# Optimization experiments

Measured on AMD Instinct MI355X. Metric: run time of the kernel, lower is better.

The kernel has to match this reference:

```python
import jax, jax.numpy as jnp
import numpy as np

N_NODES = 50000
N_PAIRS = 800000
D = 64          # node feature dim
N_BASIS = 8     # basis functions per pair


def setup_inputs() -> dict:
    key = jax.random.key(0)
    k1, k2, k3, k4, k5, k6 = jax.random.split(key, 6)
    p1 = jax.random.normal(k1, (N_NODES, D), dtype=jnp.float32)
    pair_i = jax.random.randint(k2, (N_PAIRS,), 0, N_NODES, dtype=jnp.int64)
    pair_j = jax.random.randint(k3, (N_PAIRS,), 0, N_NODES, dtype=jnp.int64)
    basis = jax.random.normal(k4, (N_PAIRS, N_BASIS), dtype=jnp.float32)
    # bias-free MLP: 64 -> 256 -> 512 (= D * N_BASIS), scaled init
    W1 = jax.random.normal(k5, (D, 256), dtype=jnp.float32) / np.sqrt(D)
    W2 = jax.random.normal(k6, (256, D * N_BASIS), dtype=jnp.float32) / np.sqrt(256.0)
    return {"p1": p1, "pair_i": pair_i, "pair_j": pair_j, "basis": basis,
            "W1": W1, "W2": W2}


def reference(p1, pair_i, pair_j, basis, W1, W2):
    # gather node features for both ends of each pair and sum -> [n_pairs, D]
    inter = p1[pair_i] + p1[pair_j]
    # bias-free FeedForward with tanh between layers
    h = jnp.tanh(inter @ W1)          # [n_pairs, 256]
    h = h @ W2                        # [n_pairs, D * N_BASIS]
    h = h.reshape(-1, p1.shape[-1], basis.shape[-1])  # [n_pairs, D, n_basis]
    out = jnp.einsum('icb,ib->ic', h, basis)          # [n_pairs, D]
    return out[:, None, :]            # [n_pairs, 1, D]
```

## Files before the change

### kernel.cpp

```cpp
#include <hip/hip_runtime.h>

typedef unsigned short u16;
typedef unsigned int   u32;
typedef __bf16 bf16x8 __attribute__((ext_vector_type(8)));
typedef float  f32x4  __attribute__((ext_vector_type(4)));
typedef float  f32x2  __attribute__((ext_vector_type(2)));
typedef unsigned short u16x8 __attribute__((ext_vector_type(8)));
typedef unsigned int   u32x2 __attribute__((ext_vector_type(2)));

#define PPB 160

__device__ __forceinline__ u16 f2bf(float f){
  union { float f; u32 i; } v; v.f = f;
  u32 u = v.i;
  u += 0x7fffu + ((u >> 16) & 1u);
  return (u16)(u >> 16);
}
__device__ __forceinline__ float tanh_fast(float x){
  x = fminf(fmaxf(x, -12.f), 12.f);
  float t = __builtin_amdgcn_exp2f(x * 2.885390081777926815f);
  return (t - 1.f) * __builtin_amdgcn_rcpf(t + 1.f);
}

__global__ __launch_bounds__(256) void transpose_cast_k(
    const float* __restrict__ in, u16* __restrict__ out, int R, int C)
{
  __shared__ u16 tile[64][65];
  const int tx = threadIdx.x & 63;
  const int ty = threadIdx.x >> 6;
  const int c0 = blockIdx.x * 64;
  const int r0 = blockIdx.y * 64;
#pragma unroll
  for (int rr = 0; rr < 16; ++rr){
    int r = ty + rr * 4;
    tile[r][tx] = f2bf(in[(size_t)(r0 + r) * C + c0 + tx]);
  }
  __syncthreads();
#pragma unroll
  for (int rr = 0; rr < 16; ++rr){
    int r = ty + rr * 4;
    out[(size_t)(c0 + r) * R + r0 + tx] = tile[tx][r];
  }
}

__global__ __launch_bounds__(256) void w2_block_k(
    const float* __restrict__ in, u16* __restrict__ out)
{
  __shared__ float tile[32][65];
  const int kk = blockIdx.x;
  const int n0 = blockIdx.y * 64;
  const int t  = threadIdx.x;
  {
    int r  = t >> 3;
    int c8 = t & 7;
    const float* src = in + (size_t)(kk*32 + r)*512 + n0 + c8*8;
    f32x4 v0 = *(const f32x4*)src;
    f32x4 v1 = *(const f32x4*)(src + 4);
#pragma unroll
    for (int e = 0; e < 4; ++e){
      tile[r][c8*8 + e]     = v0[e];
      tile[r][c8*8 + 4 + e] = v1[e];
    }
  }
  __syncthreads();
  {
    int c = t >> 2, part = t & 3;
    u16x8 o;
#pragma unroll
    for (int e = 0; e < 8; ++e) o[e] = f2bf(tile[part*8 + e][c]);
    *(u16x8*)(out + ((size_t)kk*512 + n0 + c)*32 + part*8) = o;
  }
}

__global__ __launch_bounds__(1024, 4) void pilayer_kernel(
    const float* __restrict__ p1,
    const int* __restrict__ pair_i,
    const int* __restrict__ pair_j,
    const float* __restrict__ basis,
    const u16* __restrict__ w1t,
    const u16* __restrict__ w2b,
    float* __restrict__ out,
    int n_pairs)
{
  extern __shared__ __align__(16) u16 smem[];
  u16* sh_h     = smem;
  u16* sh_inter = smem + PPB * 256;

  const int tid  = threadIdx.x;
  const int blk  = blockIdx.x;
  const int lane = tid & 63;
  const int w    = tid >> 6;
  const int m16  = lane & 15;
  const int q    = lane >> 4;
  const int sw   = m16 & 7;

  bf16x8 awf[8][2];
#pragma unroll
  for (int kk = 0; kk < 8; ++kk)
#pragma unroll
    for (int nt = 0; nt < 2; ++nt)
      awf[kk][nt] = *(const bf16x8*)(
          w2b + ((size_t)kk*512 + w*32 + nt*16 + m16)*32 + q*8);
  __builtin_amdgcn_sched_barrier(0);

  for (int u = tid; u < PPB * 8; u += 1024){
    int m   = u >> 3;
    int seg = u & 7;
    int p   = blk * PPB + m;
    if (p >= n_pairs) p = n_pairs - 1;
    const f32x4* pi = (const f32x4*)(p1 + (size_t)pair_i[p] * 64 + seg * 8);
    const f32x4* pj = (const f32x4*)(p1 + (size_t)pair_j[p] * 64 + seg * 8);
    f32x4 a0 = pi[0], a1 = pi[1];
    f32x4 c0 = pj[0], c1 = pj[1];
    u16x8 r;
#pragma unroll
    for (int e = 0; e < 4; ++e){
      r[e]     = f2bf(a0[e] + c0[e]);
      r[e + 4] = f2bf(a1[e] + c1[e]);
    }
    *(u16x8*)(sh_inter + m * 64 + ((seg ^ (m & 7)) * 8)) = r;
  }
  __syncthreads();

  {
    const u16* arow = w1t + (size_t)(w*16 + m16)*64 + q*8;
    bf16x8 af0 = *(const bf16x8*)(arow);
    bf16x8 af1 = *(const bf16x8*)(arow + 32);
    const int cw = (w*2 + (q >> 1)) ^ sw;
    for (int mt1 = 0; mt1 < PPB/16; ++mt1){
      const u16* irow = sh_inter + (size_t)(mt1*16 + m16) * 64;
      bf16x8 b0 = *(const bf16x8*)(irow + (q ^ sw) * 8);
      bf16x8 b1 = *(const bf16x8*)(irow + ((q + 4) ^ sw) * 8);
      f32x4 acc = {0.f, 0.f, 0.f, 0.f};
      acc = __builtin_amdgcn_mfma_f32_16x16x32_bf16(af0, b0, acc, 0, 0, 0);
      acc = __builtin_amdgcn_mfma_f32_16x16x32_bf16(af1, b1, acc, 0, 0, 0);
      u32 lo = (u32)f2bf(tanh_fast(acc[0])) | ((u32)f2bf(tanh_fast(acc[1])) << 16);
      u32 hi = (u32)f2bf(tanh_fast(acc[2])) | ((u32)f2bf(tanh_fast(acc[3])) << 16);
      u32x2 pk = {lo, hi};
      *(u32x2*)(sh_h + (size_t)(mt1*16 + m16)*256 + cw*8 + (q & 1)*4) = pk;
    }
  }
  __syncthreads();

  for (int mt = 0; mt < PPB/16; ++mt){
    const int row = mt*16 + m16;
    const int mg  = blk * PPB + row;
    const int mgc = (mg < n_pairs) ? mg : (n_pairs - 1);
    f32x4 bb = *(const f32x4*)(basis + (size_t)mgc*8 + (q & 1)*4);

    const u16* hbase = sh_h + (size_t)row * 256;
    f32x4 acc0 = {0.f, 0.f, 0.f, 0.f};
    f32x4 acc1 = {0.f, 0.f, 0.f, 0.f};

    bf16x8 bh = *(const bf16x8*)(hbase + (q ^ sw) * 8);
#pragma unroll
    for (int kk = 0; kk < 8; ++kk){
      bf16x8 bhn;
      if (kk < 7) bhn = *(const bf16x8*)(hbase + ((((kk + 1)*4 + q) ^ sw) * 8));
      acc0 = __builtin_amdgcn_mfma_f32_16x16x32_bf16(awf[kk][0], bh, acc0, 0, 0, 0);
      acc1 = __builtin_amdgcn_mfma_f32_16x16x32_bf16(awf[kk][1], bh, acc1, 0, 0, 0);
      bh = bhn;
    }

#pragma unroll
    for (int nt = 0; nt < 2; ++nt){
      f32x4 a = (nt == 0) ? acc0 : acc1;
      float s = a[0]*bb[0] + a[1]*bb[1] + a[2]*bb[2] + a[3]*bb[3];
      s += __shfl_xor(s, 16);
      float v2 = __shfl_xor(s, 32);
      if (q == 0 && mg < n_pairs){
        f32x2 pk = {s, v2};
        *(f32x2*)(out + (size_t)mg*64 + w*4 + nt*2) = pk;
      }
    }
  }
}

extern "C" void kernel_launch(void* const* d_in, const int* in_sizes, int n_in,
                              void* d_out, int out_size, void* d_ws, size_t ws_size,
                              hipStream_t stream)
{
  const float* p1    = (const float*)d_in[0];
  const int*   pi    = (const int*)d_in[1];
  const int*   pj    = (const int*)d_in[2];
  const float* basis = (const float*)d_in[3];
  const float* W1    = (const float*)d_in[4];
  const float* W2    = (const float*)d_in[5];
  float* out = (float*)d_out;

  u16* w1t = (u16*)d_ws;
  u16* w2b = w1t + 64 * 256;

  const int n_pairs = in_sizes[1];
  const int lds_bytes = (PPB * 256 + PPB * 64) * (int)sizeof(u16);

  static int attr_done = 0;
  if (!attr_done){
    hipFuncSetAttribute((const void*)pilayer_kernel,
                        hipFuncAttributeMaxDynamicSharedMemorySize, lds_bytes);
    attr_done = 1;
  }

  transpose_cast_k<<<dim3(4, 1), 256, 0, stream>>>(W1, w1t, 64, 256);
  w2_block_k<<<dim3(8, 8), 256, 0, stream>>>(W2, w2b);

  const int blocks = (n_pairs + PPB - 1) / PPB;
  pilayer_kernel<<<blocks, 1024, lds_bytes, stream>>>(
      p1, pi, pj, basis, w1t, w2b, out, n_pairs);
}
```

Before: 585.2 us.

## Process multiple pair chunks per block with double-buffered prefetched gathers

Each block now loops over five 128-pair chunks instead of handling one 160-pair chunk. While the second GEMM runs on the current chunk, it prefetches the next chunk's indices and node-feature gathers into a second LDS buffer. The W1 and W2 fragments held in registers are loaded once per block and reused across all chunks. The h-buffer swizzle is widened to a 4-bit XOR to reduce LDS bank conflicts. The cost is more registers for the prefetched data, an extra input buffer in LDS, and fewer blocks to hide latency with.

```diff
diff --git a/kernel.cpp b/kernel.cpp
--- a/kernel.cpp
+++ b/kernel.cpp
@@ -8,7 +8,8 @@
 typedef unsigned short u16x8 __attribute__((ext_vector_type(8)));
 typedef unsigned int   u32x2 __attribute__((ext_vector_type(2)));
 
-#define PPB 160
+#define PPB 128
+#define CPB 5
 
 __device__ __forceinline__ u16 f2bf(float f){
   union { float f; u32 i; } v; v.f = f;
@@ -83,8 +84,9 @@
     int n_pairs)
 {
   extern __shared__ __align__(16) u16 smem[];
-  u16* sh_h     = smem;
-  u16* sh_inter = smem + PPB * 256;
+  u16* sh_h  = smem;
+  u16* sh_i0 = smem + PPB * 256;
+  u16* sh_i1 = sh_i0 + PPB * 64;
 
   const int tid  = threadIdx.x;
   const int blk  = blockIdx.x;
@@ -92,7 +94,8 @@
   const int w    = tid >> 6;
   const int m16  = lane & 15;
   const int q    = lane >> 4;
-  const int sw   = m16 & 7;
+  const int sw3  = m16 & 7;
+  const int cw   = (w*2 + (q >> 1)) ^ m16;
 
   bf16x8 awf[8][2];
 #pragma unroll
@@ -101,36 +104,51 @@
     for (int nt = 0; nt < 2; ++nt)
       awf[kk][nt] = *(const bf16x8*)(
           w2b + ((size_t)kk*512 + w*32 + nt*16 + m16)*32 + q*8);
+  const u16* arow = w1t + (size_t)(w*16 + m16)*64 + q*8;
+  bf16x8 af0 = *(const bf16x8*)(arow);
+  bf16x8 af1 = *(const bf16x8*)(arow + 32);
   __builtin_amdgcn_sched_barrier(0);
 
-  for (int u = tid; u < PPB * 8; u += 1024){
-    int m   = u >> 3;
-    int seg = u & 7;
-    int p   = blk * PPB + m;
+  const int pbase = blk * CPB * PPB;
+  const int m_g   = tid >> 3;
+  const int seg_g = tid & 7;
+
+  {
+    int p = pbase + m_g;
     if (p >= n_pairs) p = n_pairs - 1;
-    const f32x4* pi = (const f32x4*)(p1 + (size_t)pair_i[p] * 64 + seg * 8);
-    const f32x4* pj = (const f32x4*)(p1 + (size_t)pair_j[p] * 64 + seg * 8);
-    f32x4 a0 = pi[0], a1 = pi[1];
-    f32x4 c0 = pj[0], c1 = pj[1];
+    const float* si = p1 + (size_t)pair_i[p]*64 + seg_g*8;
+    const float* sj = p1 + (size_t)pair_j[p]*64 + seg_g*8;
+    f32x4 a0 = ((const f32x4*)si)[0], a1 = ((const f32x4*)si)[1];
+    f32x4 b0 = ((const f32x4*)sj)[0], b1 = ((const f32x4*)sj)[1];
     u16x8 r;
 #pragma unroll
     for (int e = 0; e < 4; ++e){
-      r[e]     = f2bf(a0[e] + c0[e]);
-      r[e + 4] = f2bf(a1[e] + c1[e]);
-    }
-    *(u16x8*)(sh_inter + m * 64 + ((seg ^ (m & 7)) * 8)) = r;
+      r[e]     = f2bf(a0[e] + b0[e]);
+      r[e + 4] = f2bf(a1[e] + b1[e]);
+    }
+    *(u16x8*)(sh_i0 + m_g*64 + ((seg_g ^ (m_g & 7)) * 8)) = r;
   }
   __syncthreads();
 
-  {
-    const u16* arow = w1t + (size_t)(w*16 + m16)*64 + q*8;
-    bf16x8 af0 = *(const bf16x8*)(arow);
-    bf16x8 af1 = *(const bf16x8*)(arow + 32);
-    const int cw = (w*2 + (q >> 1)) ^ sw;
+  u16* sin_cur = sh_i0;
+  u16* sin_nxt = sh_i1;
+  int nxt_i = 0, nxt_j = 0;
+
+  for (int t = 0; t < CPB; ++t){
+    const int pb = pbase + t * PPB;
+    const bool pf = (t + 1 < CPB);
+
+    if (pf){
+      int pn = pb + PPB + m_g;
+      if (pn >= n_pairs) pn = n_pairs - 1;
+      nxt_i = pair_i[pn];
+      nxt_j = pair_j[pn];
+      asm volatile("" : "+v"(nxt_i), "+v"(nxt_j));
+    }
     for (int mt1 = 0; mt1 < PPB/16; ++mt1){
-      const u16* irow = sh_inter + (size_t)(mt1*16 + m16) * 64;
-      bf16x8 b0 = *(const bf16x8*)(irow + (q ^ sw) * 8);
-      bf16x8 b1 = *(const bf16x8*)(irow + ((q + 4) ^ sw) * 8);
+      const u16* irow = sin_cur + (size_t)(mt1*16 + m16) * 64;
+      bf16x8 b0 = *(const bf16x8*)(irow + ((q ^ sw3) * 8));
+      bf16x8 b1 = *(const bf16x8*)(irow + (((q + 4) ^ sw3) * 8));
       f32x4 acc = {0.f, 0.f, 0.f, 0.f};
       acc = __builtin_amdgcn_mfma_f32_16x16x32_bf16(af0, b0, acc, 0, 0, 0);
       acc = __builtin_amdgcn_mfma_f32_16x16x32_bf16(af1, b1, acc, 0, 0, 0);
@@ -139,40 +157,61 @@
       u32x2 pk = {lo, hi};
       *(u32x2*)(sh_h + (size_t)(mt1*16 + m16)*256 + cw*8 + (q & 1)*4) = pk;
     }
-  }
-  __syncthreads();
-
-  for (int mt = 0; mt < PPB/16; ++mt){
-    const int row = mt*16 + m16;
-    const int mg  = blk * PPB + row;
-    const int mgc = (mg < n_pairs) ? mg : (n_pairs - 1);
-    f32x4 bb = *(const f32x4*)(basis + (size_t)mgc*8 + (q & 1)*4);
-
-    const u16* hbase = sh_h + (size_t)row * 256;
-    f32x4 acc0 = {0.f, 0.f, 0.f, 0.f};
-    f32x4 acc1 = {0.f, 0.f, 0.f, 0.f};
-
-    bf16x8 bh = *(const bf16x8*)(hbase + (q ^ sw) * 8);
-#pragma unroll
-    for (int kk = 0; kk < 8; ++kk){
-      bf16x8 bhn;
-      if (kk < 7) bhn = *(const bf16x8*)(hbase + ((((kk + 1)*4 + q) ^ sw) * 8));
-      acc0 = __builtin_amdgcn_mfma_f32_16x16x32_bf16(awf[kk][0], bh, acc0, 0, 0, 0);
-      acc1 = __builtin_amdgcn_mfma_f32_16x16x32_bf16(awf[kk][1], bh, acc1, 0, 0, 0);
-      bh = bhn;
-    }
-
-#pragma unroll
-    for (int nt = 0; nt < 2; ++nt){
-      f32x4 a = (nt == 0) ? acc0 : acc1;
-      float s = a[0]*bb[0] + a[1]*bb[1] + a[2]*bb[2] + a[3]*bb[3];
-      s += __shfl_xor(s, 16);
-      float v2 = __shfl_xor(s, 32);
-      if (q == 0 && mg < n_pairs){
-        f32x2 pk = {s, v2};
-        *(f32x2*)(out + (size_t)mg*64 + w*4 + nt*2) = pk;
+    __syncthreads();
+
+    f32x4 gi0, gi1, gj0, gj1;
+    if (pf){
+      const float* si = p1 + (size_t)(u32)nxt_i*64 + seg_g*8;
+      const float* sj = p1 + (size_t)(u32)nxt_j*64 + seg_g*8;
+      gi0 = ((const f32x4*)si)[0]; gi1 = ((const f32x4*)si)[1];
+      gj0 = ((const f32x4*)sj)[0]; gj1 = ((const f32x4*)sj)[1];
+      asm volatile("" : "+v"(gi0), "+v"(gi1), "+v"(gj0), "+v"(gj1));
+    }
+
+    for (int mt = 0; mt < PPB/16; ++mt){
+      const int row = mt*16 + m16;
+      const int mg  = pb + row;
+      const int mgc = (mg < n_pairs) ? mg : (n_pairs - 1);
+      f32x4 bb = *(const f32x4*)(basis + (size_t)mgc*8 + (q & 1)*4);
+
+      const u16* hbase = sh_h + (size_t)row * 256;
+      f32x4 acc0 = {0.f, 0.f, 0.f, 0.f};
+      f32x4 acc1 = {0.f, 0.f, 0.f, 0.f};
+
+      bf16x8 bh = *(const bf16x8*)(hbase + ((q ^ m16) * 8));
+#pragma unroll
+      for (int kk = 0; kk < 8; ++kk){
+        bf16x8 bhn;
+        if (kk < 7) bhn = *(const bf16x8*)(hbase + ((((kk + 1)*4 + q) ^ m16) * 8));
+        acc0 = __builtin_amdgcn_mfma_f32_16x16x32_bf16(awf[kk][0], bh, acc0, 0, 0, 0);
+        acc1 = __builtin_amdgcn_mfma_f32_16x16x32_bf16(awf[kk][1], bh, acc1, 0, 0, 0);
+        bh = bhn;
       }
-    }
+
+#pragma unroll
+      for (int nt = 0; nt < 2; ++nt){
+        f32x4 a = (nt == 0) ? acc0 : acc1;
+        float s = a[0]*bb[0] + a[1]*bb[1] + a[2]*bb[2] + a[3]*bb[3];
+        s += __shfl_xor(s, 16);
+        float v2 = __shfl_xor(s, 32);
+        if (q == 0 && mg < n_pairs){
+          f32x2 pk = {s, v2};
+          *(f32x2*)(out + (size_t)mg*64 + w*4 + nt*2) = pk;
+        }
+      }
+    }
+
+    if (pf){
+      u16x8 r;
+#pragma unroll
+      for (int e = 0; e < 4; ++e){
+        r[e]     = f2bf(gi0[e] + gj0[e]);
+        r[e + 4] = f2bf(gi1[e] + gj1[e]);
+      }
+      *(u16x8*)(sin_nxt + m_g*64 + ((seg_g ^ (m_g & 7)) * 8)) = r;
+    }
+    __syncthreads();
+    u16* tmp = sin_cur; sin_cur = sin_nxt; sin_nxt = tmp;
   }
 }
 
@@ -192,7 +231,7 @@
   u16* w2b = w1t + 64 * 256;
 
   const int n_pairs = in_sizes[1];
-  const int lds_bytes = (PPB * 256 + PPB * 64) * (int)sizeof(u16);
+  const int lds_bytes = (PPB * 256 + 2 * PPB * 64) * (int)sizeof(u16);
 
   static int attr_done = 0;
   if (!attr_done){
@@ -204,7 +243,8 @@
   transpose_cast_k<<<dim3(4, 1), 256, 0, stream>>>(W1, w1t, 64, 256);
   w2_block_k<<<dim3(8, 8), 256, 0, stream>>>(W2, w2b);
 
-  const int blocks = (n_pairs + PPB - 1) / PPB;
+  const int n_chunks = (n_pairs + PPB - 1) / PPB;
+  const int blocks   = (n_chunks + CPB - 1) / CPB;
   pilayer_kernel<<<blocks, 1024, lds_bytes, stream>>>(
       p1, pi, pj, basis, w1t, w2b, out, n_pairs);
 }
```

Measured after the change: 680.0 us. 1.16x slower.

## Gather node features from an fp16 copy of p1 and simplify tanh/pack

Applied to the files above, without the earlier changes.

Adds a pre-pass that converts p1 to fp16 in workspace, so the per-pair gathers read half the bytes. It also uses hardware bf16 conversion for packing, drops the tanh clamp in favour of a 1-2/(t+1) form, and widens the LDS swizzle for the h buffer to a 4-bit XOR. The cost is an extra kernel pass over p1 and fp16 rounding of node features, which could overflow for large values.

```diff
diff --git a/kernel.cpp b/kernel.cpp
--- a/kernel.cpp
+++ b/kernel.cpp
@@ -3,10 +3,12 @@
 typedef unsigned short u16;
 typedef unsigned int   u32;
 typedef __bf16 bf16x8 __attribute__((ext_vector_type(8)));
+typedef _Float16 f16x8 __attribute__((ext_vector_type(8)));
 typedef float  f32x4  __attribute__((ext_vector_type(4)));
 typedef float  f32x2  __attribute__((ext_vector_type(2)));
 typedef unsigned short u16x8 __attribute__((ext_vector_type(8)));
 typedef unsigned int   u32x2 __attribute__((ext_vector_type(2)));
+typedef unsigned int   u32x4 __attribute__((ext_vector_type(4)));
 
 #define PPB 160
 
@@ -16,10 +18,30 @@
   u += 0x7fffu + ((u >> 16) & 1u);
   return (u16)(u >> 16);
 }
+__device__ __forceinline__ u32 pkbf(float lo, float hi){
+  union { __bf16 h[2]; u32 u; } v;
+  v.h[0] = (__bf16)lo; v.h[1] = (__bf16)hi;
+  return v.u;
+}
 __device__ __forceinline__ float tanh_fast(float x){
-  x = fminf(fmaxf(x, -12.f), 12.f);
   float t = __builtin_amdgcn_exp2f(x * 2.885390081777926815f);
-  return (t - 1.f) * __builtin_amdgcn_rcpf(t + 1.f);
+  return __builtin_fmaf(-2.f, __builtin_amdgcn_rcpf(t + 1.f), 1.f);
+}
+
+__global__ __launch_bounds__(256) void p1_to_f16_k(
+    const float* __restrict__ in, u16* __restrict__ out, int n8)
+{
+  int t = blockIdx.x * 256 + threadIdx.x;
+  if (t >= n8) return;
+  f32x4 v0 = *(const f32x4*)(in + (size_t)t*8);
+  f32x4 v1 = *(const f32x4*)(in + (size_t)t*8 + 4);
+  union { _Float16 h; u16 u; } c;
+  u16x8 o;
+#pragma unroll
+  for (int e = 0; e < 4; ++e){ c.h = (_Float16)v0[e]; o[e]   = c.u; }
+#pragma unroll
+  for (int e = 0; e < 4; ++e){ c.h = (_Float16)v1[e]; o[e+4] = c.u; }
+  *(u16x8*)(out + (size_t)t*8) = o;
 }
 
 __global__ __launch_bounds__(256) void transpose_cast_k(
@@ -74,6 +96,7 @@
 
 __global__ __launch_bounds__(1024, 4) void pilayer_kernel(
     const float* __restrict__ p1,
+    const u16* __restrict__ p1h,
     const int* __restrict__ pair_i,
     const int* __restrict__ pair_j,
     const float* __restrict__ basis,
@@ -92,7 +115,8 @@
   const int w    = tid >> 6;
   const int m16  = lane & 15;
   const int q    = lane >> 4;
-  const int sw   = m16 & 7;
+  const int sw3  = m16 & 7;
+  const int cw   = (w*2 + (q >> 1)) ^ m16;
 
   bf16x8 awf[8][2];
 #pragma unroll
@@ -101,44 +125,59 @@
     for (int nt = 0; nt < 2; ++nt)
       awf[kk][nt] = *(const bf16x8*)(
           w2b + ((size_t)kk*512 + w*32 + nt*16 + m16)*32 + q*8);
+  const u16* arow = w1t + (size_t)(w*16 + m16)*64 + q*8;
+  bf16x8 af0 = *(const bf16x8*)(arow);
+  bf16x8 af1 = *(const bf16x8*)(arow + 32);
   __builtin_amdgcn_sched_barrier(0);
 
-  for (int u = tid; u < PPB * 8; u += 1024){
-    int m   = u >> 3;
-    int seg = u & 7;
-    int p   = blk * PPB + m;
-    if (p >= n_pairs) p = n_pairs - 1;
-    const f32x4* pi = (const f32x4*)(p1 + (size_t)pair_i[p] * 64 + seg * 8);
-    const f32x4* pj = (const f32x4*)(p1 + (size_t)pair_j[p] * 64 + seg * 8);
-    f32x4 a0 = pi[0], a1 = pi[1];
-    f32x4 c0 = pj[0], c1 = pj[1];
-    u16x8 r;
-#pragma unroll
-    for (int e = 0; e < 4; ++e){
-      r[e]     = f2bf(a0[e] + c0[e]);
-      r[e + 4] = f2bf(a1[e] + c1[e]);
-    }
-    *(u16x8*)(sh_inter + m * 64 + ((seg ^ (m & 7)) * 8)) = r;
-  }
-  __syncthreads();
-
-  {
-    const u16* arow = w1t + (size_t)(w*16 + m16)*64 + q*8;
-    bf16x8 af0 = *(const bf16x8*)(arow);
-    bf16x8 af1 = *(const bf16x8*)(arow + 32);
-    const int cw = (w*2 + (q >> 1)) ^ sw;
-    for (int mt1 = 0; mt1 < PPB/16; ++mt1){
-      const u16* irow = sh_inter + (size_t)(mt1*16 + m16) * 64;
-      bf16x8 b0 = *(const bf16x8*)(irow + (q ^ sw) * 8);
-      bf16x8 b1 = *(const bf16x8*)(irow + ((q + 4) ^ sw) * 8);
-      f32x4 acc = {0.f, 0.f, 0.f, 0.f};
-      acc = __builtin_amdgcn_mfma_f32_16x16x32_bf16(af0, b0, acc, 0, 0, 0);
-      acc = __builtin_amdgcn_mfma_f32_16x16x32_bf16(af1, b1, acc, 0, 0, 0);
-      u32 lo = (u32)f2bf(tanh_fast(acc[0])) | ((u32)f2bf(tanh_fast(acc[1])) << 16);
-      u32 hi = (u32)f2bf(tanh_fast(acc[2])) | ((u32)f2bf(tanh_fast(acc[3])) << 16);
-      u32x2 pk = {lo, hi};
-      *(u32x2*)(sh_h + (size_t)(mt1*16 + m16)*256 + cw*8 + (q & 1)*4) = pk;
-    }
+  if (p1h != nullptr){
+    for (int u = tid; u < PPB * 8; u += 1024){
+      int m   = u >> 3;
+      int seg = u & 7;
+      int p   = blk * PPB + m;
+      if (p >= n_pairs) p = n_pairs - 1;
+      union { u16x8 u; f16x8 h; } vi, vj;
+      vi.u = *(const u16x8*)(p1h + (size_t)pair_i[p]*64 + seg*8);
+      vj.u = *(const u16x8*)(p1h + (size_t)pair_j[p]*64 + seg*8);
+      u32x4 o;
+#pragma unroll
+      for (int e = 0; e < 4; ++e)
+        o[e] = pkbf((float)vi.h[2*e]   + (float)vj.h[2*e],
+                    (float)vi.h[2*e+1] + (float)vj.h[2*e+1]);
+      *(u32x4*)(sh_inter + m*64 + ((seg ^ (m & 7)) * 8)) = o;
+    }
+  } else {
+    for (int u = tid; u < PPB * 8; u += 1024){
+      int m   = u >> 3;
+      int seg = u & 7;
+      int p   = blk * PPB + m;
+      if (p >= n_pairs) p = n_pairs - 1;
+      const f32x4* pi = (const f32x4*)(p1 + (size_t)pair_i[p]*64 + seg*8);
+      const f32x4* pj = (const f32x4*)(p1 + (size_t)pair_j[p]*64 + seg*8);
+      f32x4 a0 = pi[0], a1 = pi[1];
+      f32x4 b0 = pj[0], b1 = pj[1];
+      u32x4 o;
+#pragma unroll
+      for (int e = 0; e < 2; ++e){
+        o[e]   = pkbf(a0[2*e] + b0[2*e], a0[2*e+1] + b0[2*e+1]);
+        o[e+2] = pkbf(a1[2*e] + b1[2*e], a1[2*e+1] + b1[2*e+1]);
+      }
+      *(u32x4*)(sh_inter + m*64 + ((seg ^ (m & 7)) * 8)) = o;
+    }
+  }
+  __syncthreads();
+
+  for (int mt1 = 0; mt1 < PPB/16; ++mt1){
+    const u16* irow = sh_inter + (size_t)(mt1*16 + m16) * 64;
+    bf16x8 b0 = *(const bf16x8*)(irow + ((q ^ sw3) * 8));
+    bf16x8 b1 = *(const bf16x8*)(irow + (((q + 4) ^ sw3) * 8));
+    f32x4 acc = {0.f, 0.f, 0.f, 0.f};
+    acc = __builtin_amdgcn_mfma_f32_16x16x32_bf16(af0, b0, acc, 0, 0, 0);
+    acc = __builtin_amdgcn_mfma_f32_16x16x32_bf16(af1, b1, acc, 0, 0, 0);
+    u32x2 pk;
+    pk[0] = pkbf(tanh_fast(acc[0]), tanh_fast(acc[1]));
+    pk[1] = pkbf(tanh_fast(acc[2]), tanh_fast(acc[3]));
+    *(u32x2*)(sh_h + (size_t)(mt1*16 + m16)*256 + cw*8 + (q & 1)*4) = pk;
   }
   __syncthreads();
 
@@ -152,11 +191,11 @@
     f32x4 acc0 = {0.f, 0.f, 0.f, 0.f};
     f32x4 acc1 = {0.f, 0.f, 0.f, 0.f};
 
-    bf16x8 bh = *(const bf16x8*)(hbase + (q ^ sw) * 8);
+    bf16x8 bh = *(const bf16x8*)(hbase + ((q ^ m16) * 8));
 #pragma unroll
     for (int kk = 0; kk < 8; ++kk){
       bf16x8 bhn;
-      if (kk < 7) bhn = *(const bf16x8*)(hbase + ((((kk + 1)*4 + q) ^ sw) * 8));
+      if (kk < 7) bhn = *(const bf16x8*)(hbase + ((((kk + 1)*4 + q) ^ m16) * 8));
       acc0 = __builtin_amdgcn_mfma_f32_16x16x32_bf16(awf[kk][0], bh, acc0, 0, 0, 0);
       acc1 = __builtin_amdgcn_mfma_f32_16x16x32_bf16(awf[kk][1], bh, acc1, 0, 0, 0);
       bh = bhn;
@@ -188,10 +227,15 @@
   const float* W2    = (const float*)d_in[5];
   float* out = (float*)d_out;
 
+  const int n_pairs = in_sizes[1];
+  const int n_nodes = in_sizes[0] / 64;
+
   u16* w1t = (u16*)d_ws;
   u16* w2b = w1t + 64 * 256;
-
-  const int n_pairs = in_sizes[1];
+  u16* p1h = w2b + 8 * 512 * 32;
+  const size_t need = (size_t)(64*256 + 8*512*32 + n_nodes*64) * sizeof(u16);
+  const bool use_h = (ws_size >= need);
+
   const int lds_bytes = (PPB * 256 + PPB * 64) * (int)sizeof(u16);
 
   static int attr_done = 0;
@@ -203,8 +247,12 @@
 
   transpose_cast_k<<<dim3(4, 1), 256, 0, stream>>>(W1, w1t, 64, 256);
   w2_block_k<<<dim3(8, 8), 256, 0, stream>>>(W2, w2b);
+  if (use_h){
+    const int n8 = n_nodes * 8;
+    p1_to_f16_k<<<(n8 + 255)/256, 256, 0, stream>>>(p1, p1h, n8);
+  }
 
   const int blocks = (n_pairs + PPB - 1) / PPB;
   pilayer_kernel<<<blocks, 1024, lds_bytes, stream>>>(
-      p1, pi, pj, basis, w1t, w2b, out, n_pairs);
-}
+      p1, use_h ? p1h : nullptr, pi, pj, basis, w1t, w2b, out, n_pairs);
+}
```

Measured after the change: 567.9 us. -3.0%, faster.
